# Kernel tuning notes

Hardware: AMD Instinct MI355X
Metric: run time of the kernel (lower is better)

The kernel has to match this reference:

```python
import jax, jax.numpy as jnp
import numpy as np

# MambaConfig defaults for d_model=512
N_LAYERS = 2
D_MODEL = 512
ED = 2 * D_MODEL        # d_inner (expand_factor=2)
D_STATE = 16
D_CONV = 4
DT_RANK = D_MODEL // 16  # 32
INPUT_DIM = 64
EPS = 1e-5


def silu(v):
    return v * jax.nn.sigmoid(v)


def rmsnorm(v, w):
    return v * jax.lax.rsqrt(jnp.mean(v * v, axis=-1, keepdims=True) + EPS) * w


def setup_inputs() -> dict:
    key = jax.random.key(0)
    ks = jax.random.split(key, 12)
    B, L = 2, 2048
    s = 0.02
    x = jax.random.normal(ks[0], (B, L, INPUT_DIM), dtype=jnp.float32)
    emb_w = jax.random.normal(ks[1], (D_MODEL, INPUT_DIM), dtype=jnp.float32) * s
    emb_b = jnp.zeros((D_MODEL,), dtype=jnp.float32)
    in_proj_w = jax.random.normal(ks[2], (N_LAYERS, 2 * ED, D_MODEL), dtype=jnp.float32) * s
    conv_w = jax.random.normal(ks[3], (N_LAYERS, ED, D_CONV), dtype=jnp.float32) * 0.2
    conv_b = jax.random.normal(ks[4], (N_LAYERS, ED), dtype=jnp.float32) * 0.02
    x_proj_w = jax.random.normal(ks[5], (N_LAYERS, DT_RANK + 2 * D_STATE, ED), dtype=jnp.float32) * s
    dt_proj_w = jax.random.normal(ks[6], (N_LAYERS, ED, DT_RANK), dtype=jnp.float32) * s
    dt_proj_b = jax.random.normal(ks[7], (N_LAYERS, ED), dtype=jnp.float32) * 0.5 - 4.0  # softplus(~-4) ~ small dt
    A_log = jnp.log(jnp.tile(jnp.arange(1, D_STATE + 1, dtype=jnp.float32), (N_LAYERS, ED, 1)))  # S4D-real init
    D = jnp.ones((N_LAYERS, ED), dtype=jnp.float32)
    out_proj_w = jax.random.normal(ks[8], (N_LAYERS, D_MODEL, ED), dtype=jnp.float32) * s
    norm_w = jnp.ones((N_LAYERS, D_MODEL), dtype=jnp.float32)
    return dict(x=x, emb_w=emb_w, emb_b=emb_b, in_proj_w=in_proj_w, conv_w=conv_w,
                conv_b=conv_b, x_proj_w=x_proj_w, dt_proj_w=dt_proj_w, dt_proj_b=dt_proj_b,
                A_log=A_log, D=D, out_proj_w=out_proj_w, norm_w=norm_w)


def mamba_block(h, in_w, cw, cb, xp_w, dt_w, dt_b, a_log, d_param, out_w):
    B, L, _ = h.shape
    xz = jnp.einsum('bld,ed->ble', h, in_w)            # (B,L,2*ED)
    xi, z = jnp.split(xz, 2, axis=-1)
    # depthwise causal conv along L
    xc = jax.lax.conv_general_dilated(
        xi.transpose(0, 2, 1), cw[:, None, :], (1,), ((D_CONV - 1, 0),),
        dimension_numbers=('NCH', 'OIH', 'NCH'), feature_group_count=ED)
    xi = silu(xc.transpose(0, 2, 1) + cb)              # (B,L,ED)
    dbc = jnp.einsum('ble,ke->blk', xi, xp_w)          # (B,L,dt_rank+2N)
    dt, Bm, Cm = jnp.split(dbc, [DT_RANK, DT_RANK + D_STATE], axis=-1)
    delta = jax.nn.softplus(jnp.einsum('blr,er->ble', dt, dt_w) + dt_b)  # (B,L,ED)
    A = -jnp.exp(a_log)                                # (ED,N)
    dA = jnp.exp(delta[..., None] * A)                 # (B,L,ED,N)
    dBx = (delta * xi)[..., None] * Bm[:, :, None, :]  # (B,L,ED,N)

    def step(hs, inp):
        dA_t, dBx_t, C_t = inp
        hs = dA_t * hs + dBx_t                          # (B,ED,N)
        y_t = jnp.einsum('ben,bn->be', hs, C_t)
        return hs, y_t

    h0 = jnp.zeros((B, ED, D_STATE), dtype=h.dtype)
    _, ys = jax.lax.scan(step, h0, (dA.transpose(1, 0, 2, 3),
                                    dBx.transpose(1, 0, 2, 3),
                                    Cm.transpose(1, 0, 2)))
    y = ys.transpose(1, 0, 2) + d_param * xi
    y = y * silu(z)
    return jnp.einsum('ble,de->bld', y, out_w)


def reference(x, emb_w, emb_b, in_proj_w, conv_w, conv_b, x_proj_w,
              dt_proj_w, dt_proj_b, A_log, D, out_proj_w, norm_w):
    h = jnp.einsum('bli,di->bld', x, emb_w) + emb_b
    for i in range(N_LAYERS):
        h = h + mamba_block(rmsnorm(h, norm_w[i]), in_proj_w[i], conv_w[i], conv_b[i],
                            x_proj_w[i], dt_proj_w[i], dt_proj_b[i],
                            A_log[i], D[i], out_proj_w[i])
    return h
```

## Files before the change

kernel.cpp:

```cpp
#include <hip/hip_runtime.h>
#include <hip/hip_bf16.h>

#define TOKENS   4096
#define BATCH    2
#define LSEQ     2048
#define DM       512
#define EDIM     1024
#define NSTATE   16
#define DCONV    4
#define DTRANK   32
#define TCHUNK   32
#define NCHUNKS  (LSEQ/TCHUNK)
#define KSPLIT   8

typedef unsigned short u16;
typedef __attribute__((ext_vector_type(8))) short bf16x8;
typedef __attribute__((ext_vector_type(8))) unsigned short u16x8;
typedef __attribute__((ext_vector_type(4))) float f32x4;

#define ASYNC_CP16(gptr, lptr) \
    __builtin_amdgcn_global_load_lds((const __attribute__((address_space(1))) void*)(gptr), \
                                     (__attribute__((address_space(3))) void*)(lptr), 16, 0, 0)

__device__ __forceinline__ u16 f2b(float f){
    union{float f; unsigned u;} v; v.f=f;
    unsigned r = v.u + 0x7FFFu + ((v.u>>16)&1u);
    return (u16)(r>>16);
}
__device__ __forceinline__ float b2f(u16 b){
    union{unsigned u; float f;} v; v.u = ((unsigned)b)<<16; return v.f;
}

template<bool BF>
__device__ __forceinline__ float ld(const void* p, long i) {
    if (BF) return b2f(((const u16*)p)[i]);
    return ((const float*)p)[i];
}
__device__ __forceinline__ float ldf(const void* p, long i, int bf){
    return bf ? b2f(((const u16*)p)[i]) : ((const float*)p)[i];
}

__device__ __forceinline__ float sigmoidf_(float v){ return 1.f/(1.f+__expf(-v)); }
__device__ __forceinline__ float siluf_(float v){ return v*sigmoidf_(v); }
__device__ __forceinline__ float softplusf_(float v){ return v>20.f ? v : __logf(1.f + __expf(v)); }

__global__ void detect_kernel(const void* probe, int* flag){
    unsigned u = *(const unsigned*)probe;
    *flag = (u == 0x3F800000u) ? 0 : 1;
}

__global__ void convall_kernel(const void* s0, u16* d0, long n0,
                               const void* s1, u16* d1, long n1,
                               const void* s2, u16* d2, long n2,
                               const void* s3, u16* d3, long n3,
                               const void* s4, u16* d4, long n4,
                               const int* flag){
    if (*flag) return;
    long ntot = n0+n1+n2+n3+n4;
    for (long i = (long)blockIdx.x*256 + threadIdx.x; i < ntot; i += (long)gridDim.x*256){
        long j = i;
        if (j < n0){ d0[j] = f2b(((const float*)s0)[j]); continue; } j -= n0;
        if (j < n1){ d1[j] = f2b(((const float*)s1)[j]); continue; } j -= n1;
        if (j < n2){ d2[j] = f2b(((const float*)s2)[j]); continue; } j -= n2;
        if (j < n3){ d3[j] = f2b(((const float*)s3)[j]); continue; } j -= n3;
        d4[j] = f2b(((const float*)s4)[j]);
    }
}

template<bool BF>
__device__ void rms_body(const float* h, const void* nw, u16* hn, int layer){
    int wv = threadIdx.x>>6, lane = threadIdx.x&63;
    int t = blockIdx.x*4 + wv;
    long base = (long)t*DM + lane*8;
    float4 a = *(const float4*)&h[base];
    float4 b = *(const float4*)&h[base+4];
    float s = a.x*a.x+a.y*a.y+a.z*a.z+a.w*a.w + b.x*b.x+b.y*b.y+b.z*b.z+b.w*b.w;
    #pragma unroll
    for (int off=1; off<64; off<<=1) s += __shfl_xor(s, off);
    float scale = rsqrtf(s*(1.0f/DM) + 1e-5f);
    float v[8] = {a.x,a.y,a.z,a.w,b.x,b.y,b.z,b.w};
    u16x8 o;
    #pragma unroll
    for (int j=0;j<8;j++) o[j] = f2b(v[j]*scale*ld<BF>(nw, (long)layer*DM + lane*8 + j));
    *(u16x8*)&hn[base] = o;
}
__global__ void rms_kernel(const float* h, const void* nw, u16* hn, int layer, const int* flag){
    if (*flag) rms_body<true>(h,nw,hn,layer); else rms_body<false>(h,nw,hn,layer);
}

template<int MODE>
__global__ __launch_bounds__(256,2)
void gemm128_kernel(const void* Aorig, const u16* __restrict__ Aconv,
                    const void* worig, const u16* __restrict__ wconv,
                    void* Cv, const void* bias, const float* __restrict__ resid,
                    int M, int N, int K, int lda, long boff, const int* flag){
    int bf = *flag;
    const u16* A = bf ? (const u16*)Aorig : Aconv;
    const u16* W = bf ? ((const u16*)worig) + boff : wconv + boff;
    __shared__ u16 As[128*32];
    __shared__ u16 Bs[128*32];
    int t = threadIdx.x;
    int n0 = blockIdx.x*128, m0 = blockIdx.y*128;
    int w = t>>6, lane = t&63;
    int wm = w>>1, wn = w&1;
    int lm = lane&15, lk = lane>>4;
    int srow = w*16 + (lane>>2);
    int seg8 = (lane&3)*8;
    u16* lbaseA1 = As + w*512;
    u16* lbaseA2 = As + 2048 + w*512;
    u16* lbaseB1 = Bs + w*512;
    u16* lbaseB2 = Bs + 2048 + w*512;
    f32x4 acc[4][4];
    #pragma unroll
    for (int i=0;i<4;i++)
        #pragma unroll
        for (int j=0;j<4;j++) acc[i][j] = (f32x4){0.f,0.f,0.f,0.f};
    for (int k0=0; k0<K; k0+=32){
        __syncthreads();
        ASYNC_CP16(&A[(long)(m0+srow)*lda + k0 + seg8],      lbaseA1);
        ASYNC_CP16(&A[(long)(m0+64+srow)*lda + k0 + seg8],   lbaseA2);
        ASYNC_CP16(&W[(long)(n0+srow)*K + k0 + seg8],        lbaseB1);
        ASYNC_CP16(&W[(long)(n0+64+srow)*K + k0 + seg8],     lbaseB2);
        __syncthreads();
        bf16x8 af[4], bfr[4];
        #pragma unroll
        for (int mi=0;mi<4;mi++) af[mi]  = *(const bf16x8*)&As[(wm*64+mi*16+lm)*32 + lk*8];
        #pragma unroll
        for (int ni=0;ni<4;ni++) bfr[ni] = *(const bf16x8*)&Bs[(wn*64+ni*16+lm)*32 + lk*8];
        #pragma unroll
        for (int mi=0;mi<4;mi++)
            #pragma unroll
            for (int ni=0;ni<4;ni++)
                acc[mi][ni] = __builtin_amdgcn_mfma_f32_16x16x32_bf16(af[mi], bfr[ni], acc[mi][ni], 0,0,0);
    }
    #pragma unroll
    for (int mi=0;mi<4;mi++){
        #pragma unroll
        for (int ni=0;ni<4;ni++){
            int row = m0 + wm*64 + mi*16 + lk*4;
            int col = n0 + wn*64 + ni*16 + lm;
            float bb = (MODE==0) ? ldf(bias, col, bf) : 0.f;
            #pragma unroll
            for (int r=0;r<4;r++){
                long idx = (long)(row+r)*N + col;
                if (MODE==0) ((float*)Cv)[idx] = acc[mi][ni][r] + bb;
                if (MODE==1) ((u16*)Cv)[idx]   = f2b(acc[mi][ni][r]);
                if (MODE==2) ((float*)Cv)[idx] += acc[mi][ni][r];
                if (MODE==3){
                    float v = resid[idx] + acc[mi][ni][r];
                    if (bf) ((u16*)Cv)[idx] = f2b(v);
                    else    ((float*)Cv)[idx] = v;
                }
            }
        }
    }
}

__global__ __launch_bounds__(256,2)
void gemmx_kernel(const u16* __restrict__ A, const void* worig, const u16* __restrict__ wconv,
                  float* __restrict__ part, long boff, const int* flag){
    const u16* W = (*flag) ? ((const u16*)worig) + boff : wconv + boff;
    __shared__ u16 As[128*40];
    __shared__ u16 Bs[64*40];
    int t = threadIdx.x;
    int m0 = blockIdx.x*128;
    int kz = blockIdx.y;
    int w = t>>6, lane = t&63;
    int wm = w>>1, wn = w&1;
    int lm = lane&15, lk = lane>>4;
    f32x4 acc[4][2];
    #pragma unroll
    for (int i=0;i<4;i++){ acc[i][0]=(f32x4){0,0,0,0}; acc[i][1]=(f32x4){0,0,0,0}; }
    int arow = t>>1;
    int aks  = (t&1)*16;
    const int KS = EDIM/KSPLIT;
    for (int it=0; it<KS; it+=32){
        int k0 = kz*KS + it;
        float4 av0 = *(const float4*)&A[(long)(m0+arow)*EDIM + k0 + aks];
        float4 av1 = *(const float4*)&A[(long)(m0+arow)*EDIM + k0 + aks + 8];
        float4 bv0, bv1;
        if (t < 128){
            bv0 = *(const float4*)&W[(long)arow*EDIM + k0 + aks];
            bv1 = *(const float4*)&W[(long)arow*EDIM + k0 + aks + 8];
        }
        __syncthreads();
        *(float4*)&As[arow*40 + aks]     = av0;
        *(float4*)&As[arow*40 + aks + 8] = av1;
        if (t < 128){
            *(float4*)&Bs[arow*40 + aks]     = bv0;
            *(float4*)&Bs[arow*40 + aks + 8] = bv1;
        }
        __syncthreads();
        bf16x8 af[4], bfr[2];
        #pragma unroll
        for (int mi=0;mi<4;mi++) af[mi]  = *(const bf16x8*)&As[(wm*64+mi*16+lm)*40 + lk*8];
        #pragma unroll
        for (int ni=0;ni<2;ni++) bfr[ni] = *(const bf16x8*)&Bs[(wn*32+ni*16+lm)*40 + lk*8];
        #pragma unroll
        for (int mi=0;mi<4;mi++)
            #pragma unroll
            for (int ni=0;ni<2;ni++)
                acc[mi][ni] = __builtin_amdgcn_mfma_f32_16x16x32_bf16(af[mi], bfr[ni], acc[mi][ni], 0,0,0);
    }
    #pragma unroll
    for (int mi=0;mi<4;mi++){
        #pragma unroll
        for (int ni=0;ni<2;ni++){
            int row = m0 + wm*64 + mi*16 + lk*4;
            int col = wn*32 + ni*16 + lm;
            #pragma unroll
            for (int r=0;r<4;r++)
                part[((long)kz*TOKENS + row + r)*64 + col] = acc[mi][ni][r];
        }
    }
}

__global__ void reduce_dbc_kernel(const float* __restrict__ part, float* __restrict__ dbc){
    long i = ((long)blockIdx.x*256 + threadIdx.x)*4;
    float4 s = *(const float4*)&part[i];
    #pragma unroll
    for (int z=1; z<KSPLIT; z++){
        float4 p = *(const float4*)&part[(long)z*TOKENS*64 + i];
        s.x += p.x; s.y += p.y; s.z += p.z; s.w += p.w;
    }
    *(float4*)&dbc[i] = s;
}

template<bool BF>
__device__ void conv_body(const u16* xz, const void* cw, const void* cb, u16* xic, int layer){
    long idx = (long)blockIdx.x*256 + threadIdx.x;
    int t = (int)(idx >> 7), e0 = (int)((idx & 127)*8);
    int l = t & (LSEQ-1);
    u16x8 r0 = {0,0,0,0,0,0,0,0}, r1 = r0, r2 = r0;
    if (l >= 3) r0 = *(const u16x8*)&xz[(long)(t-3)*2048 + e0];
    if (l >= 2) r1 = *(const u16x8*)&xz[(long)(t-2)*2048 + e0];
    if (l >= 1) r2 = *(const u16x8*)&xz[(long)(t-1)*2048 + e0];
    u16x8 r3 = *(const u16x8*)&xz[(long)t*2048 + e0];
    u16x8 o;
    #pragma unroll
    for (int j=0;j<8;j++){
        int e = e0 + j;
        long wo = ((long)layer*EDIM + e)*DCONV;
        float s = ld<BF>(cb, (long)layer*EDIM + e);
        s = fmaf(b2f(r0[j]), ld<BF>(cw,wo+0), s);
        s = fmaf(b2f(r1[j]), ld<BF>(cw,wo+1), s);
        s = fmaf(b2f(r2[j]), ld<BF>(cw,wo+2), s);
        s = fmaf(b2f(r3[j]), ld<BF>(cw,wo+3), s);
        o[j] = f2b(siluf_(s));
    }
    *(u16x8*)&xic[(long)t*EDIM + e0] = o;
}
__global__ void conv_kernel(const u16* xz, const void* cw, const void* cb, u16* xic, int layer, const int* flag){
    if (*flag) conv_body<true>(xz,cw,cb,xic,layer); else conv_body<false>(xz,cw,cb,xic,layer);
}

template<bool BF>
__device__ void phase1_body(const float* __restrict__ dbc, const u16* __restrict__ xic,
                            const void* A_log, const void* dtw, const void* dtb,
                            float* __restrict__ chunkP, float* __restrict__ chunkL, int layer){
    int lane = threadIdx.x;
    int ch = blockIdx.x*64 + lane;
    int b = ch >> 10, e = ch & (EDIM-1);
    int c = blockIdx.y;
    float w[DTRANK];
    long wo = ((long)layer*EDIM + e)*DTRANK;
    #pragma unroll
    for (int r=0;r<DTRANK;r++) w[r] = ld<BF>(dtw, wo+r);
    float bias = ld<BF>(dtb, (long)layer*EDIM + e);
    float a[NSTATE];
    long ao = ((long)layer*EDIM + e)*NSTATE;
    #pragma unroll
    for (int n=0;n<NSTATE;n++) a[n] = -__expf(ld<BF>(A_log, ao+n));
    float P[NSTATE], L[NSTATE];
    #pragma unroll
    for (int n=0;n<NSTATE;n++){ P[n]=1.f; L[n]=0.f; }
    long tok0 = (long)b*LSEQ + (long)c*TCHUNK;
    for (int i=0;i<TCHUNK;i++){
        long tok = tok0 + i;
        const float4* row4 = (const float4*)(dbc + tok*64);
        float rr[DTRANK];
        #pragma unroll
        for (int q=0;q<8;q++){ float4 v=row4[q]; rr[q*4]=v.x; rr[q*4+1]=v.y; rr[q*4+2]=v.z; rr[q*4+3]=v.w; }
        float Bv[NSTATE];
        #pragma unroll
        for (int q=0;q<4;q++){ float4 v=row4[8+q]; Bv[q*4]=v.x; Bv[q*4+1]=v.y; Bv[q*4+2]=v.z; Bv[q*4+3]=v.w; }
        float s = bias;
        #pragma unroll
        for (int r=0;r<DTRANK;r++) s = fmaf(rr[r], w[r], s);
        float delta = softplusf_(s);
        float xv = b2f(xic[tok*EDIM + e]);
        float dx = delta * xv;
        #pragma unroll
        for (int n=0;n<NSTATE;n++){
            float dA = __expf(delta * a[n]);
            P[n] *= dA;
            L[n] = fmaf(dA, L[n], dx * Bv[n]);
        }
    }
    long g = ((long)b*NCHUNKS + c)*EDIM*NSTATE + (long)e*NSTATE;
    #pragma unroll
    for (int n=0;n<NSTATE;n+=4){
        *(float4*)&chunkP[g+n] = make_float4(P[n],P[n+1],P[n+2],P[n+3]);
        *(float4*)&chunkL[g+n] = make_float4(L[n],L[n+1],L[n+2],L[n+3]);
    }
}
__global__ void phase1_kernel(const float* dbc, const u16* xic, const void* A_log,
                              const void* dtw, const void* dtb,
                              float* chunkP, float* chunkL, int layer, const int* flag){
    if (*flag) phase1_body<true>(dbc,xic,A_log,dtw,dtb,chunkP,chunkL,layer);
    else       phase1_body<false>(dbc,xic,A_log,dtw,dtb,chunkP,chunkL,layer);
}

__global__ void phase2_kernel(float* chunkP, const float* __restrict__ chunkL){
    int tid = blockIdx.x*256 + threadIdx.x;
    int q  = (tid & 3)*4;
    int ch = tid >> 2;
    int b = ch >> 10, e = ch & (EDIM-1);
    float4 h = make_float4(0,0,0,0);
    for (int c=0;c<NCHUNKS;c++){
        long g = ((long)(b*NCHUNKS + c)*EDIM + e)*NSTATE + q;
        float4 P = *(const float4*)&chunkP[g];
        float4 L = *(const float4*)&chunkL[g];
        *(float4*)&chunkP[g] = h;
        h.x = fmaf(P.x, h.x, L.x);
        h.y = fmaf(P.y, h.y, L.y);
        h.z = fmaf(P.z, h.z, L.z);
        h.w = fmaf(P.w, h.w, L.w);
    }
}

template<bool BF>
__device__ void phase3_body(const float* __restrict__ dbc, const u16* __restrict__ xic,
                            const u16* __restrict__ xzb, u16* __restrict__ ybf,
                            const float* __restrict__ chunkP,
                            const void* A_log, const void* dtw, const void* dtb,
                            const void* Dp, int layer){
    int lane = threadIdx.x;
    int ch = blockIdx.x*64 + lane;
    int b = ch >> 10, e = ch & (EDIM-1);
    int c = blockIdx.y;
    float w[DTRANK];
    long wo = ((long)layer*EDIM + e)*DTRANK;
    #pragma unroll
    for (int r=0;r<DTRANK;r++) w[r] = ld<BF>(dtw, wo+r);
    float bias = ld<BF>(dtb, (long)layer*EDIM + e);
    float a[NSTATE];
    long ao = ((long)layer*EDIM + e)*NSTATE;
    #pragma unroll
    for (int n=0;n<NSTATE;n++) a[n] = -__expf(ld<BF>(A_log, ao+n));
    float D_e = ld<BF>(Dp, (long)layer*EDIM + e);
    float h[NSTATE];
    long g = ((long)b*NCHUNKS + c)*EDIM*NSTATE + (long)e*NSTATE;
    #pragma unroll
    for (int q=0;q<NSTATE;q+=4){
        float4 v = *(const float4*)&chunkP[g+q];
        h[q]=v.x; h[q+1]=v.y; h[q+2]=v.z; h[q+3]=v.w;
    }
    long tok0 = (long)b*LSEQ + (long)c*TCHUNK;
    for (int i=0;i<TCHUNK;i++){
        long tok = tok0 + i;
        const float4* row4 = (const float4*)(dbc + tok*64);
        float rr[DTRANK];
        #pragma unroll
        for (int q=0;q<8;q++){ float4 v=row4[q]; rr[q*4]=v.x; rr[q*4+1]=v.y; rr[q*4+2]=v.z; rr[q*4+3]=v.w; }
        float Bv[NSTATE], Cv[NSTATE];
        #pragma unroll
        for (int q=0;q<4;q++){ float4 v=row4[8+q];  Bv[q*4]=v.x; Bv[q*4+1]=v.y; Bv[q*4+2]=v.z; Bv[q*4+3]=v.w; }
        #pragma unroll
        for (int q=0;q<4;q++){ float4 v=row4[12+q]; Cv[q*4]=v.x; Cv[q*4+1]=v.y; Cv[q*4+2]=v.z; Cv[q*4+3]=v.w; }
        float s = bias;
        #pragma unroll
        for (int r=0;r<DTRANK;r++) s = fmaf(rr[r], w[r], s);
        float delta = softplusf_(s);
        float xv = b2f(xic[tok*EDIM + e]);
        float zv = b2f(xzb[tok*2048 + EDIM + e]);
        float dx = delta * xv;
        float acc = D_e * xv;
        #pragma unroll
        for (int n=0;n<NSTATE;n++){
            float dA = __expf(delta * a[n]);
            h[n] = fmaf(dA, h[n], dx * Bv[n]);
            acc = fmaf(h[n], Cv[n], acc);
        }
        ybf[tok*EDIM + e] = f2b(acc * siluf_(zv));
    }
}
__global__ void phase3_kernel(const float* dbc, const u16* xic, const u16* xzb, u16* ybf,
                              const float* chunkP, const void* A_log, const void* dtw,
                              const void* dtb, const void* Dp, int layer, const int* flag){
    if (*flag) phase3_body<true>(dbc,xic,xzb,ybf,chunkP,A_log,dtw,dtb,Dp,layer);
    else       phase3_body<false>(dbc,xic,xzb,ybf,chunkP,A_log,dtw,dtb,Dp,layer);
}

extern "C" void kernel_launch(void* const* d_in, const int* in_sizes, int n_in,
                              void* d_out, int out_size, void* d_ws, size_t ws_size,
                              hipStream_t stream){
    const void* x       = d_in[0];
    const void* emb_w   = d_in[1];
    const void* emb_b   = d_in[2];
    const void* in_w    = d_in[3];
    const void* conv_w  = d_in[4];
    const void* conv_b  = d_in[5];
    const void* xp_w    = d_in[6];
    const void* dt_w    = d_in[7];
    const void* dt_b    = d_in[8];
    const void* A_log   = d_in[9];
    const void* Dp      = d_in[10];
    const void* out_w   = d_in[11];
    const void* norm_w  = d_in[12];

    const long N_X   = (long)TOKENS*64;
    const long N_EW  = (long)DM*64;
    const long N_IN  = (long)2*2*EDIM*DM;
    const long N_XP  = (long)2*64*EDIM;
    const long N_OUT = (long)2*DM*EDIM;

    char* ws = (char*)d_ws;
    int*   flag    = (int*)ws;
    float* h       = (float*)(ws + 256);
    u16*   hn      = (u16*)  (h      + (long)TOKENS*DM);
    u16*   xzb     = hn      + (long)TOKENS*DM;
    u16*   xic     = xzb     + (long)TOKENS*2*EDIM;
    u16*   ybf     = xic     + (long)TOKENS*EDIM;
    float* dbc     = (float*)(ybf + (long)TOKENS*EDIM);
    float* dpart   = dbc     + (long)TOKENS*64;
    float* chunkP  = dpart   + (long)KSPLIT*TOKENS*64;
    float* chunkL  = chunkP  + (long)BATCH*NCHUNKS*EDIM*NSTATE;
    u16*   w_in    = (u16*)  (chunkL + (long)BATCH*NCHUNKS*EDIM*NSTATE);
    u16*   w_xp    = w_in    + N_IN;
    u16*   w_out   = w_xp    + N_XP;
    u16*   x_cv    = w_out   + N_OUT;
    u16*   ew_cv   = x_cv    + N_X;

    detect_kernel<<<1, 1, 0, stream>>>(norm_w, flag);
    convall_kernel<<<4096, 256, 0, stream>>>(
        x, x_cv, N_X,  emb_w, ew_cv, N_EW,  in_w, w_in, N_IN,
        xp_w, w_xp, N_XP,  out_w, w_out, N_OUT,  flag);

    gemm128_kernel<0><<<dim3(DM/128, TOKENS/128), 256, 0, stream>>>(
        x, x_cv, emb_w, ew_cv, h, emb_b, nullptr, TOKENS, DM, 64, 64, 0, flag);

    for (int layer = 0; layer < 2; layer++){
        rms_kernel<<<TOKENS/4, 256, 0, stream>>>(h, norm_w, hn, layer, flag);

        gemm128_kernel<1><<<dim3(2*EDIM/128, TOKENS/128), 256, 0, stream>>>(
            hn, hn, in_w, w_in, xzb, nullptr, nullptr,
            TOKENS, 2*EDIM, DM, DM, (long)layer*2*EDIM*DM, flag);

        conv_kernel<<<(TOKENS*EDIM)/(256*8), 256, 0, stream>>>(xzb, conv_w, conv_b, xic, layer, flag);

        gemmx_kernel<<<dim3(TOKENS/128, KSPLIT), 256, 0, stream>>>(
            xic, xp_w, w_xp, dpart, (long)layer*64*EDIM, flag);
        reduce_dbc_kernel<<<(TOKENS*64)/(256*4), 256, 0, stream>>>(dpart, dbc);

        phase1_kernel<<<dim3((BATCH*EDIM)/64, NCHUNKS), 64, 0, stream>>>(
            dbc, xic, A_log, dt_w, dt_b, chunkP, chunkL, layer, flag);
        phase2_kernel<<<(BATCH*EDIM*4)/256, 256, 0, stream>>>(chunkP, chunkL);
        phase3_kernel<<<dim3((BATCH*EDIM)/64, NCHUNKS), 64, 0, stream>>>(
            dbc, xic, xzb, ybf, chunkP, A_log, dt_w, dt_b, Dp, layer, flag);

        if (layer == 0){
            gemm128_kernel<2><<<dim3(DM/128, TOKENS/128), 256, 0, stream>>>(
                ybf, ybf, out_w, w_out, h, nullptr, nullptr,
                TOKENS, DM, EDIM, EDIM, 0L, flag);
        } else {
            gemm128_kernel<3><<<dim3(DM/128, TOKENS/128), 256, 0, stream>>>(
                ybf, ybf, out_w, w_out, d_out, nullptr, h,
                TOKENS, DM, EDIM, EDIM, (long)DM*EDIM, flag);
        }
    }
}
```

Baseline: 423.7 us.

## Precompute delta via MFMA GEMM, halve scan chunk, prefetch scan inputs

Adds a bf16 MFMA GEMM, with a fused bias and softplus epilogue, that computes delta for all tokens and channels once into a bf16 buffer. The per-channel 32-wide dot product was previously recomputed in both scan phase1 and phase3. The scan chunk length drops from 32 to 16, which doubles the number of chunks for more parallelism but makes the sequential phase2 pass longer. Phase1, phase2 and phase3 now software-prefetch the next step's inputs. Rounding delta and the dt inputs to bf16 adds some precision loss.

```diff
diff --git a/kernel.cpp b/kernel.cpp
--- a/kernel.cpp
+++ b/kernel.cpp
@@ -9,13 +9,14 @@
 #define NSTATE   16
 #define DCONV    4
 #define DTRANK   32
-#define TCHUNK   32
+#define TCHUNK   16
 #define NCHUNKS  (LSEQ/TCHUNK)
 #define KSPLIT   8
 
 typedef unsigned short u16;
 typedef __attribute__((ext_vector_type(8))) short bf16x8;
 typedef __attribute__((ext_vector_type(8))) unsigned short u16x8;
+typedef __attribute__((ext_vector_type(4))) unsigned short u16x4;
 typedef __attribute__((ext_vector_type(4))) float f32x4;
 
 #define ASYNC_CP16(gptr, lptr) \
@@ -54,16 +55,18 @@
                                const void* s2, u16* d2, long n2,
                                const void* s3, u16* d3, long n3,
                                const void* s4, u16* d4, long n4,
+                               const void* s5, u16* d5, long n5,
                                const int* flag){
     if (*flag) return;
-    long ntot = n0+n1+n2+n3+n4;
+    long ntot = n0+n1+n2+n3+n4+n5;
     for (long i = (long)blockIdx.x*256 + threadIdx.x; i < ntot; i += (long)gridDim.x*256){
         long j = i;
         if (j < n0){ d0[j] = f2b(((const float*)s0)[j]); continue; } j -= n0;
         if (j < n1){ d1[j] = f2b(((const float*)s1)[j]); continue; } j -= n1;
         if (j < n2){ d2[j] = f2b(((const float*)s2)[j]); continue; } j -= n2;
         if (j < n3){ d3[j] = f2b(((const float*)s3)[j]); continue; } j -= n3;
-        d4[j] = f2b(((const float*)s4)[j]);
+        if (j < n4){ d4[j] = f2b(((const float*)s4)[j]); continue; } j -= n4;
+        d5[j] = f2b(((const float*)s5)[j]);
     }
 }
 
@@ -92,7 +95,7 @@
 __global__ __launch_bounds__(256,2)
 void gemm128_kernel(const void* Aorig, const u16* __restrict__ Aconv,
                     const void* worig, const u16* __restrict__ wconv,
-                    void* Cv, const void* bias, const float* __restrict__ resid,
+                    void* Cv, const void* bias, long bias_off, const float* __restrict__ resid,
                     int M, int N, int K, int lda, long boff, const int* flag){
     int bf = *flag;
     const u16* A = bf ? (const u16*)Aorig : Aconv;
@@ -139,7 +142,7 @@
         for (int ni=0;ni<4;ni++){
             int row = m0 + wm*64 + mi*16 + lk*4;
             int col = n0 + wn*64 + ni*16 + lm;
-            float bb = (MODE==0) ? ldf(bias, col, bf) : 0.f;
+            float bb = (MODE==0 || MODE==4) ? ldf(bias, bias_off + col, bf) : 0.f;
             #pragma unroll
             for (int r=0;r<4;r++){
                 long idx = (long)(row+r)*N + col;
@@ -151,6 +154,7 @@
                     if (bf) ((u16*)Cv)[idx] = f2b(v);
                     else    ((float*)Cv)[idx] = v;
                 }
+                if (MODE==4) ((u16*)Cv)[idx] = f2b(softplusf_(acc[mi][ni][r] + bb));
             }
         }
     }
@@ -215,7 +219,8 @@
     }
 }
 
-__global__ void reduce_dbc_kernel(const float* __restrict__ part, float* __restrict__ dbc){
+__global__ void reduce_dbc_kernel(const float* __restrict__ part, float* __restrict__ dbc,
+                                  u16* __restrict__ dbc16){
     long i = ((long)blockIdx.x*256 + threadIdx.x)*4;
     float4 s = *(const float4*)&part[i];
     #pragma unroll
@@ -224,6 +229,8 @@
         s.x += p.x; s.y += p.y; s.z += p.z; s.w += p.w;
     }
     *(float4*)&dbc[i] = s;
+    u16x4 o; o[0]=f2b(s.x); o[1]=f2b(s.y); o[2]=f2b(s.z); o[3]=f2b(s.w);
+    *(u16x4*)&dbc16[i] = o;
 }
 
 template<bool BF>
@@ -255,18 +262,13 @@
 }
 
 template<bool BF>
-__device__ void phase1_body(const float* __restrict__ dbc, const u16* __restrict__ xic,
-                            const void* A_log, const void* dtw, const void* dtb,
+__device__ void phase1_body(const float* __restrict__ dbc, const u16* __restrict__ delt,
+                            const u16* __restrict__ xic, const void* A_log,
                             float* __restrict__ chunkP, float* __restrict__ chunkL, int layer){
     int lane = threadIdx.x;
     int ch = blockIdx.x*64 + lane;
     int b = ch >> 10, e = ch & (EDIM-1);
     int c = blockIdx.y;
-    float w[DTRANK];
-    long wo = ((long)layer*EDIM + e)*DTRANK;
-    #pragma unroll
-    for (int r=0;r<DTRANK;r++) w[r] = ld<BF>(dtw, wo+r);
-    float bias = ld<BF>(dtb, (long)layer*EDIM + e);
     float a[NSTATE];
     long ao = ((long)layer*EDIM + e)*NSTATE;
     #pragma unroll
@@ -275,24 +277,26 @@
     #pragma unroll
     for (int n=0;n<NSTATE;n++){ P[n]=1.f; L[n]=0.f; }
     long tok0 = (long)b*LSEQ + (long)c*TCHUNK;
+    float de = b2f(delt[tok0*EDIM + e]);
+    float xv = b2f(xic[tok0*EDIM + e]);
+    const float4* r4 = (const float4*)(dbc + tok0*64);
+    float4 B0 = r4[8], B1 = r4[9], B2 = r4[10], B3 = r4[11];
     for (int i=0;i<TCHUNK;i++){
-        long tok = tok0 + i;
-        const float4* row4 = (const float4*)(dbc + tok*64);
-        float rr[DTRANK];
-        #pragma unroll
-        for (int q=0;q<8;q++){ float4 v=row4[q]; rr[q*4]=v.x; rr[q*4+1]=v.y; rr[q*4+2]=v.z; rr[q*4+3]=v.w; }
-        float Bv[NSTATE];
-        #pragma unroll
-        for (int q=0;q<4;q++){ float4 v=row4[8+q]; Bv[q*4]=v.x; Bv[q*4+1]=v.y; Bv[q*4+2]=v.z; Bv[q*4+3]=v.w; }
-        float s = bias;
-        #pragma unroll
-        for (int r=0;r<DTRANK;r++) s = fmaf(rr[r], w[r], s);
-        float delta = softplusf_(s);
-        float xv = b2f(xic[tok*EDIM + e]);
-        float dx = delta * xv;
+        float de_c=de, xv_c=xv;
+        float4 b0=B0, b1=B1, b2=B2, b3=B3;
+        if (i+1 < TCHUNK){
+            long t2 = tok0 + i + 1;
+            de = b2f(delt[t2*EDIM + e]);
+            xv = b2f(xic[t2*EDIM + e]);
+            const float4* n4 = (const float4*)(dbc + t2*64);
+            B0=n4[8]; B1=n4[9]; B2=n4[10]; B3=n4[11];
+        }
+        float Bv[NSTATE] = {b0.x,b0.y,b0.z,b0.w, b1.x,b1.y,b1.z,b1.w,
+                            b2.x,b2.y,b2.z,b2.w, b3.x,b3.y,b3.z,b3.w};
+        float dx = de_c * xv_c;
         #pragma unroll
         for (int n=0;n<NSTATE;n++){
-            float dA = __expf(delta * a[n]);
+            float dA = __expf(de_c * a[n]);
             P[n] *= dA;
             L[n] = fmaf(dA, L[n], dx * Bv[n]);
         }
@@ -304,11 +308,10 @@
         *(float4*)&chunkL[g+n] = make_float4(L[n],L[n+1],L[n+2],L[n+3]);
     }
 }
-__global__ void phase1_kernel(const float* dbc, const u16* xic, const void* A_log,
-                              const void* dtw, const void* dtb,
+__global__ void phase1_kernel(const float* dbc, const u16* delt, const u16* xic, const void* A_log,
                               float* chunkP, float* chunkL, int layer, const int* flag){
-    if (*flag) phase1_body<true>(dbc,xic,A_log,dtw,dtb,chunkP,chunkL,layer);
-    else       phase1_body<false>(dbc,xic,A_log,dtw,dtb,chunkP,chunkL,layer);
+    if (*flag) phase1_body<true>(dbc,delt,xic,A_log,chunkP,chunkL,layer);
+    else       phase1_body<false>(dbc,delt,xic,A_log,chunkP,chunkL,layer);
 }
 
 __global__ void phase2_kernel(float* chunkP, const float* __restrict__ chunkL){
@@ -317,33 +320,34 @@
     int ch = tid >> 2;
     int b = ch >> 10, e = ch & (EDIM-1);
     float4 h = make_float4(0,0,0,0);
+    long g0 = ((long)(b*NCHUNKS)*EDIM + e)*NSTATE + q;
+    float4 P = *(const float4*)&chunkP[g0];
+    float4 L = *(const float4*)&chunkL[g0];
     for (int c=0;c<NCHUNKS;c++){
         long g = ((long)(b*NCHUNKS + c)*EDIM + e)*NSTATE + q;
-        float4 P = *(const float4*)&chunkP[g];
-        float4 L = *(const float4*)&chunkL[g];
+        float4 Pc = P, Lc = L;
+        if (c+1 < NCHUNKS){
+            long g2 = g + (long)EDIM*NSTATE;
+            P = *(const float4*)&chunkP[g2];
+            L = *(const float4*)&chunkL[g2];
+        }
         *(float4*)&chunkP[g] = h;
-        h.x = fmaf(P.x, h.x, L.x);
-        h.y = fmaf(P.y, h.y, L.y);
-        h.z = fmaf(P.z, h.z, L.z);
-        h.w = fmaf(P.w, h.w, L.w);
+        h.x = fmaf(Pc.x, h.x, Lc.x);
+        h.y = fmaf(Pc.y, h.y, Lc.y);
+        h.z = fmaf(Pc.z, h.z, Lc.z);
+        h.w = fmaf(Pc.w, h.w, Lc.w);
     }
 }
 
 template<bool BF>
-__device__ void phase3_body(const float* __restrict__ dbc, const u16* __restrict__ xic,
-                            const u16* __restrict__ xzb, u16* __restrict__ ybf,
-                            const float* __restrict__ chunkP,
-                            const void* A_log, const void* dtw, const void* dtb,
-                            const void* Dp, int layer){
+__device__ void phase3_body(const float* __restrict__ dbc, const u16* __restrict__ delt,
+                            const u16* __restrict__ xic, const u16* __restrict__ xzb,
+                            u16* __restrict__ ybf, const float* __restrict__ chunkP,
+                            const void* A_log, const void* Dp, int layer){
     int lane = threadIdx.x;
     int ch = blockIdx.x*64 + lane;
     int b = ch >> 10, e = ch & (EDIM-1);
     int c = blockIdx.y;
-    float w[DTRANK];
-    long wo = ((long)layer*EDIM + e)*DTRANK;
-    #pragma unroll
-    for (int r=0;r<DTRANK;r++) w[r] = ld<BF>(dtw, wo+r);
-    float bias = ld<BF>(dtb, (long)layer*EDIM + e);
     float a[NSTATE];
     long ao = ((long)layer*EDIM + e)*NSTATE;
     #pragma unroll
@@ -357,39 +361,45 @@
         h[q]=v.x; h[q+1]=v.y; h[q+2]=v.z; h[q+3]=v.w;
     }
     long tok0 = (long)b*LSEQ + (long)c*TCHUNK;
+    float de = b2f(delt[tok0*EDIM + e]);
+    float xv = b2f(xic[tok0*EDIM + e]);
+    float zv = b2f(xzb[tok0*2048 + EDIM + e]);
+    const float4* r4 = (const float4*)(dbc + tok0*64);
+    float4 B0=r4[8], B1=r4[9], B2=r4[10], B3=r4[11];
+    float4 C0=r4[12], C1=r4[13], C2=r4[14], C3=r4[15];
     for (int i=0;i<TCHUNK;i++){
         long tok = tok0 + i;
-        const float4* row4 = (const float4*)(dbc + tok*64);
-        float rr[DTRANK];
-        #pragma unroll
-        for (int q=0;q<8;q++){ float4 v=row4[q]; rr[q*4]=v.x; rr[q*4+1]=v.y; rr[q*4+2]=v.z; rr[q*4+3]=v.w; }
-        float Bv[NSTATE], Cv[NSTATE];
-        #pragma unroll
-        for (int q=0;q<4;q++){ float4 v=row4[8+q];  Bv[q*4]=v.x; Bv[q*4+1]=v.y; Bv[q*4+2]=v.z; Bv[q*4+3]=v.w; }
-        #pragma unroll
-        for (int q=0;q<4;q++){ float4 v=row4[12+q]; Cv[q*4]=v.x; Cv[q*4+1]=v.y; Cv[q*4+2]=v.z; Cv[q*4+3]=v.w; }
-        float s = bias;
-        #pragma unroll
-        for (int r=0;r<DTRANK;r++) s = fmaf(rr[r], w[r], s);
-        float delta = softplusf_(s);
-        float xv = b2f(xic[tok*EDIM + e]);
-        float zv = b2f(xzb[tok*2048 + EDIM + e]);
-        float dx = delta * xv;
-        float acc = D_e * xv;
+        float de_c=de, xv_c=xv, zv_c=zv;
+        float4 b0=B0,b1=B1,b2=B2,b3=B3, c0=C0,c1=C1,c2=C2,c3=C3;
+        if (i+1 < TCHUNK){
+            long t2 = tok + 1;
+            de = b2f(delt[t2*EDIM + e]);
+            xv = b2f(xic[t2*EDIM + e]);
+            zv = b2f(xzb[t2*2048 + EDIM + e]);
+            const float4* n4 = (const float4*)(dbc + t2*64);
+            B0=n4[8]; B1=n4[9]; B2=n4[10]; B3=n4[11];
+            C0=n4[12]; C1=n4[13]; C2=n4[14]; C3=n4[15];
+        }
+        float Bv[NSTATE] = {b0.x,b0.y,b0.z,b0.w, b1.x,b1.y,b1.z,b1.w,
+                            b2.x,b2.y,b2.z,b2.w, b3.x,b3.y,b3.z,b3.w};
+        float Cv[NSTATE] = {c0.x,c0.y,c0.z,c0.w, c1.x,c1.y,c1.z,c1.w,
+                            c2.x,c2.y,c2.z,c2.w, c3.x,c3.y,c3.z,c3.w};
+        float dx = de_c * xv_c;
+        float acc = D_e * xv_c;
         #pragma unroll
         for (int n=0;n<NSTATE;n++){
-            float dA = __expf(delta * a[n]);
+            float dA = __expf(de_c * a[n]);
             h[n] = fmaf(dA, h[n], dx * Bv[n]);
             acc = fmaf(h[n], Cv[n], acc);
         }
-        ybf[tok*EDIM + e] = f2b(acc * siluf_(zv));
-    }
-}
-__global__ void phase3_kernel(const float* dbc, const u16* xic, const u16* xzb, u16* ybf,
-                              const float* chunkP, const void* A_log, const void* dtw,
-                              const void* dtb, const void* Dp, int layer, const int* flag){
-    if (*flag) phase3_body<true>(dbc,xic,xzb,ybf,chunkP,A_log,dtw,dtb,Dp,layer);
-    else       phase3_body<false>(dbc,xic,xzb,ybf,chunkP,A_log,dtw,dtb,Dp,layer);
+        ybf[tok*EDIM + e] = f2b(acc * siluf_(zv_c));
+    }
+}
+__global__ void phase3_kernel(const float* dbc, const u16* delt, const u16* xic, const u16* xzb,
+                              u16* ybf, const float* chunkP, const void* A_log,
+                              const void* Dp, int layer, const int* flag){
+    if (*flag) phase3_body<true>(dbc,delt,xic,xzb,ybf,chunkP,A_log,Dp,layer);
+    else       phase3_body<false>(dbc,delt,xic,xzb,ybf,chunkP,A_log,Dp,layer);
 }
 
 extern "C" void kernel_launch(void* const* d_in, const int* in_sizes, int n_in,
@@ -414,6 +424,7 @@
     const long N_IN  = (long)2*2*EDIM*DM;
     const long N_XP  = (long)2*64*EDIM;
     const long N_OUT = (long)2*DM*EDIM;
+    const long N_DT  = (long)2*EDIM*DTRANK;
 
     char* ws = (char*)d_ws;
     int*   flag    = (int*)ws;
@@ -422,50 +433,57 @@
     u16*   xzb     = hn      + (long)TOKENS*DM;
     u16*   xic     = xzb     + (long)TOKENS*2*EDIM;
     u16*   ybf     = xic     + (long)TOKENS*EDIM;
-    float* dbc     = (float*)(ybf + (long)TOKENS*EDIM);
-    float* dpart   = dbc     + (long)TOKENS*64;
+    u16*   deltab  = ybf     + (long)TOKENS*EDIM;
+    float* dbc     = (float*)(deltab + (long)TOKENS*EDIM);
+    u16*   dbc16   = (u16*)  (dbc + (long)TOKENS*64);
+    float* dpart   = (float*)(dbc16 + (long)TOKENS*64);
     float* chunkP  = dpart   + (long)KSPLIT*TOKENS*64;
     float* chunkL  = chunkP  + (long)BATCH*NCHUNKS*EDIM*NSTATE;
     u16*   w_in    = (u16*)  (chunkL + (long)BATCH*NCHUNKS*EDIM*NSTATE);
     u16*   w_xp    = w_in    + N_IN;
     u16*   w_out   = w_xp    + N_XP;
-    u16*   x_cv    = w_out   + N_OUT;
+    u16*   w_dt    = w_out   + N_OUT;
+    u16*   x_cv    = w_dt    + N_DT;
     u16*   ew_cv   = x_cv    + N_X;
 
     detect_kernel<<<1, 1, 0, stream>>>(norm_w, flag);
     convall_kernel<<<4096, 256, 0, stream>>>(
         x, x_cv, N_X,  emb_w, ew_cv, N_EW,  in_w, w_in, N_IN,
-        xp_w, w_xp, N_XP,  out_w, w_out, N_OUT,  flag);
+        xp_w, w_xp, N_XP,  out_w, w_out, N_OUT,  dt_w, w_dt, N_DT,  flag);
 
     gemm128_kernel<0><<<dim3(DM/128, TOKENS/128), 256, 0, stream>>>(
-        x, x_cv, emb_w, ew_cv, h, emb_b, nullptr, TOKENS, DM, 64, 64, 0, flag);
+        x, x_cv, emb_w, ew_cv, h, emb_b, 0L, nullptr, TOKENS, DM, 64, 64, 0, flag);
 
     for (int layer = 0; layer < 2; layer++){
         rms_kernel<<<TOKENS/4, 256, 0, stream>>>(h, norm_w, hn, layer, flag);
 
         gemm128_kernel<1><<<dim3(2*EDIM/128, TOKENS/128), 256, 0, stream>>>(
-            hn, hn, in_w, w_in, xzb, nullptr, nullptr,
+            hn, hn, in_w, w_in, xzb, nullptr, 0L, nullptr,
             TOKENS, 2*EDIM, DM, DM, (long)layer*2*EDIM*DM, flag);
 
         conv_kernel<<<(TOKENS*EDIM)/(256*8), 256, 0, stream>>>(xzb, conv_w, conv_b, xic, layer, flag);
 
         gemmx_kernel<<<dim3(TOKENS/128, KSPLIT), 256, 0, stream>>>(
             xic, xp_w, w_xp, dpart, (long)layer*64*EDIM, flag);
-        reduce_dbc_kernel<<<(TOKENS*64)/(256*4), 256, 0, stream>>>(dpart, dbc);
+        reduce_dbc_kernel<<<(TOKENS*64)/(256*4), 256, 0, stream>>>(dpart, dbc, dbc16);
+
+        gemm128_kernel<4><<<dim3(EDIM/128, TOKENS/128), 256, 0, stream>>>(
+            dbc16, dbc16, dt_w, w_dt, deltab, dt_b, (long)layer*EDIM, nullptr,
+            TOKENS, EDIM, DTRANK, 64, (long)layer*EDIM*DTRANK, flag);
 
         phase1_kernel<<<dim3((BATCH*EDIM)/64, NCHUNKS), 64, 0, stream>>>(
-            dbc, xic, A_log, dt_w, dt_b, chunkP, chunkL, layer, flag);
+            dbc, deltab, xic, A_log, chunkP, chunkL, layer, flag);
         phase2_kernel<<<(BATCH*EDIM*4)/256, 256, 0, stream>>>(chunkP, chunkL);
         phase3_kernel<<<dim3((BATCH*EDIM)/64, NCHUNKS), 64, 0, stream>>>(
-            dbc, xic, xzb, ybf, chunkP, A_log, dt_w, dt_b, Dp, layer, flag);
+            dbc, deltab, xic, xzb, ybf, chunkP, A_log, Dp, layer, flag);
 
         if (layer == 0){
             gemm128_kernel<2><<<dim3(DM/128, TOKENS/128), 256, 0, stream>>>(
-                ybf, ybf, out_w, w_out, h, nullptr, nullptr,
+                ybf, ybf, out_w, w_out, h, nullptr, 0L, nullptr,
                 TOKENS, DM, EDIM, EDIM, 0L, flag);
         } else {
             gemm128_kernel<3><<<dim3(DM/128, TOKENS/128), 256, 0, stream>>>(
-                ybf, ybf, out_w, w_out, d_out, nullptr, h,
+                ybf, ybf, out_w, w_out, d_out, nullptr, 0L, h,
                 TOKENS, DM, EDIM, EDIM, (long)DM*EDIM, flag);
         }
     }
```

Result: no change. 419.0 us (-1.1%).
